# Kernel optimization log

Hardware: AMD Instinct MI355X
Metric: run time of the kernel (lower is better)

## Reference

```python
import jax, jax.numpy as jnp
import numpy as np

# dims: V vocab, D embed, C classes, S seq, L layers, M proj_dim (random features), B batch
V, D, C, S, L, M, B = 32000, 512, 2, 2048, 4, 64, 16
H = 4 * D  # FFN hidden


def setup_inputs() -> dict:
    key = jax.random.key(0)
    ks = jax.random.split(key, 16)
    sc = 0.02
    n = lambda k, shape, s=sc: jax.random.normal(k, shape, jnp.float32) * s
    return {
        'x': jax.random.randint(ks[0], (B, S), 0, V),
        'embed': n(ks[1], (V, D)),
        'pos': n(ks[2], (S, D)),
        'Wq': n(ks[3], (L, D, D)), 'bq': jnp.zeros((L, D), jnp.float32),
        'Wk': n(ks[4], (L, D, D)), 'bk': jnp.zeros((L, D), jnp.float32),
        'Wv': n(ks[5], (L, D, D)), 'bv': jnp.zeros((L, D), jnp.float32),
        'P': jax.random.normal(ks[6], (L, D, M), jnp.float32) / np.sqrt(D),  # Performer random-feature projection
        'Wo': n(ks[7], (L, D, D)), 'bo': jnp.zeros((L, D), jnp.float32),
        'ln_g': jnp.ones((L, D), jnp.float32), 'ln_b': jnp.zeros((L, D), jnp.float32),
        'W1': n(ks[8], (L, D, H)), 'b1': jnp.zeros((L, H), jnp.float32),
        'W2': n(ks[9], (L, H, D)), 'b2': jnp.zeros((L, D), jnp.float32),
        'Wc1': n(ks[10], (D, D // 2)), 'bc1': jnp.zeros((D // 2,), jnp.float32),
        'Wc2': n(ks[11], (D // 2, C)), 'bc2': jnp.zeros((C,), jnp.float32),
    }


def _layernorm(x, g, b, eps=1e-5):
    mu = x.mean(-1, keepdims=True)
    var = ((x - mu) ** 2).mean(-1, keepdims=True)
    return (x - mu) * jax.lax.rsqrt(var + eps) * g + b


def reference(x, embed, pos, Wq, bq, Wk, bk, Wv, bv, P, Wo, bo,
              ln_g, ln_b, W1, b1, W2, b2, Wc1, bc1, Wc2, bc2):
    # token embedding + learned positional embedding
    h = embed[x] + pos[None, :, :]  # [B,S,D]
    for l in range(L):
        r = h
        # Performer linear attention
        q = h @ Wq[l] + bq[l]
        k = h @ Wk[l] + bk[l]
        v = h @ Wv[l] + bv[l]
        pq = jax.nn.elu(q @ P[l]) + 1.0  # [B,S,M] positive feature map
        pk = jax.nn.elu(k @ P[l]) + 1.0
        kv = jnp.einsum('bsm,bsd->bmd', pk, v)              # associative K^T V reduction
        z = jnp.einsum('bsm,bm->bs', pq, pk.sum(axis=1)) + 1e-6
        att = jnp.einsum('bsm,bmd->bsd', pq, kv) / z[..., None]
        att = att @ Wo[l] + bo[l]
        # LayerNorm -> FFN (dropout is identity in eval)
        hn = _layernorm(att, ln_g[l], ln_b[l])
        ff = jax.nn.gelu(hn @ W1[l] + b1[l], approximate=False) @ W2[l] + b2[l]
        h = ff + r  # residual around the whole Sequential block
    pooled = h[:, 0, :]  # CLS pooling
    hid = jax.nn.relu(pooled @ Wc1 + bc1)
    return hid @ Wc2 + bc2  # [B,C] logits
```

## Files before the change

kernel.cpp:

```cpp
#include <hip/hip_runtime.h>
#include <hip/hip_bf16.h>
#include <math.h>

constexpr int kV = 32000;
constexpr int kD = 512;
constexpr int kC = 2;
constexpr int kS = 2048;
constexpr int kL = 4;
constexpr int kM = 64;
constexpr int kB = 16;
constexpr int kH = 2048;
constexpr int kBS = kB * kS;

typedef __hip_bfloat16 bf16;
using bf16x8 = __attribute__((ext_vector_type(8))) short;
using f32x4  = __attribute__((ext_vector_type(4))) float;

#define GLOBAL_LOAD_LDS16(gp, lp)                                              \
  __builtin_amdgcn_global_load_lds(                                            \
      (const __attribute__((address_space(1))) void*)(gp),                     \
      (__attribute__((address_space(3))) void*)(lp), 16, 0, 0)

__device__ inline unsigned short f2bf_u16(float f) {
  bf16 b = __float2bfloat16(f);
  return *reinterpret_cast<unsigned short*>(&b);
}

__device__ inline float fast_gelu(float v) {
  float y  = v * 0.70710678118654752f;
  float ay = fabsf(y);
  float t  = __builtin_amdgcn_rcpf(fmaf(0.3275911f, ay, 1.0f));
  float e  = __expf(-y * y);
  float p  = fmaf(1.061405429f, t, -1.453152027f);
  p = fmaf(p, t, 1.421413741f);
  p = fmaf(p, t, -0.284496736f);
  p = fmaf(p, t, 0.254829592f);
  float er = fmaf(-p * t, e, 1.0f);
  er = copysignf(er, y);
  return 0.5f * v * (1.0f + er);
}

__global__ __launch_bounds__(256) void embed_kernel(const int* __restrict__ x,
    const float* __restrict__ emb, const float* __restrict__ pos,
    float* __restrict__ h, bf16* __restrict__ hb) {
  int tid = blockIdx.x * 256 + threadIdx.x;
  int row = tid >> 7;
  int d4  = tid & 127;
  int tok = x[row];
  int s   = row & (kS - 1);
  float4 e = ((const float4*)emb)[(size_t)tok * 128 + d4];
  float4 p = ((const float4*)pos)[(size_t)s * 128 + d4];
  float4 o;
  o.x = e.x + p.x; o.y = e.y + p.y; o.z = e.z + p.z; o.w = e.w + p.w;
  ((float4*)h)[(size_t)row * 128 + d4] = o;
  ushort4 ub;
  ub.x = f2bf_u16(o.x); ub.y = f2bf_u16(o.y);
  ub.z = f2bf_u16(o.z); ub.w = f2bf_u16(o.w);
  ((ushort4*)hb)[(size_t)row * 128 + d4] = ub;
}

__global__ __launch_bounds__(256) void transpose_cast_kernel(
    const float* __restrict__ W, bf16* __restrict__ Wt, int K, int N) {
  __shared__ float tile[32][33];
  const int k0 = blockIdx.x * 32, n0 = blockIdx.y * 32;
  int tx = threadIdx.x & 31, ty = threadIdx.x >> 5;
#pragma unroll
  for (int i = 0; i < 32; i += 8)
    tile[ty + i][tx] = W[(size_t)(k0 + ty + i) * N + n0 + tx];
  __syncthreads();
#pragma unroll
  for (int i = 0; i < 32; i += 8)
    Wt[(size_t)(n0 + ty + i) * K + k0 + tx] = __float2bfloat16(tile[tx][ty + i]);
}

__global__ __launch_bounds__(256) void cast_bf16_kernel(
    const float* __restrict__ src, bf16* __restrict__ dst) {
  int gid = blockIdx.x * 256 + threadIdx.x;
  float4 v = ((const float4*)src)[gid];
  ushort4 u;
  u.x = f2bf_u16(v.x); u.y = f2bf_u16(v.y);
  u.z = f2bf_u16(v.z); u.w = f2bf_u16(v.w);
  ((ushort4*)dst)[gid] = u;
}

__global__ __launch_bounds__(256) void zero512_kernel(float* __restrict__ p) {
  if (threadIdx.x < 128) ((float4*)p)[threadIdx.x] = make_float4(0.f, 0.f, 0.f, 0.f);
}

__global__ __launch_bounds__(256) void wfold_dual_kernel(
    const float* __restrict__ Wq, const float* __restrict__ Wk,
    const float* __restrict__ P, bf16* __restrict__ Wqpt,
    bf16* __restrict__ Wkpt) {
  int gid = blockIdx.x * 256 + threadIdx.x;
  const float* W = (gid < 32768) ? Wq : Wk;
  bf16* out      = (gid < 32768) ? Wqpt : Wkpt;
  int id = gid & 32767;
  int m  = id & 63;
  int kk = id >> 6;
  float a0 = 0.f, a1 = 0.f, a2 = 0.f, a3 = 0.f;
#pragma unroll 4
  for (int c = 0; c < kD; c += 4) {
    float4 w = *(const float4*)&W[(size_t)kk * kD + c];
    a0 = fmaf(w.x, P[(size_t)(c + 0) * kM + m], a0);
    a1 = fmaf(w.y, P[(size_t)(c + 1) * kM + m], a1);
    a2 = fmaf(w.z, P[(size_t)(c + 2) * kM + m], a2);
    a3 = fmaf(w.w, P[(size_t)(c + 3) * kM + m], a3);
  }
  out[(size_t)m * kD + kk] = __float2bfloat16((a0 + a1) + (a2 + a3));
}

__global__ __launch_bounds__(128) void bfold_kernel(const float* __restrict__ bq,
    const float* __restrict__ bk, const float* __restrict__ P,
    float* __restrict__ bqp, float* __restrict__ bkp) {
  int m = threadIdx.x & (kM - 1);
  const float* src = (threadIdx.x >> 6) ? bk : bq;
  float* dst = (threadIdx.x >> 6) ? bkp : bqp;
  float acc = 0.f;
  for (int c = 0; c < kD; ++c) acc += src[c] * P[(size_t)c * kM + m];
  dst[m] = acc;
}

__global__ __launch_bounds__(256) void bvwo_kernel(const float* __restrict__ bv,
    const float* __restrict__ Wo, float* __restrict__ bvWo) {
  __shared__ float part[4][64];
  int d0 = blockIdx.x * 64;
  int dc = threadIdx.x & 63;
  int eg = threadIdx.x >> 6;
  float acc = 0.f;
  int e0 = eg * 128;
#pragma unroll 4
  for (int e = e0; e < e0 + 128; ++e)
    acc = fmaf(bv[e], Wo[(size_t)e * kD + d0 + dc], acc);
  part[eg][dc] = acc;
  __syncthreads();
  if (eg == 0)
    bvWo[d0 + dc] = (part[0][dc] + part[1][dc]) + (part[2][dc] + part[3][dc]);
}

template <int BK, int BN, int ACT, bool HAS_RES, bool HAS_OUTER, bool WRITE_F32, bool WRITE_BF16>
__global__ __launch_bounds__(256) void mfma_gemm(
    const bf16* __restrict__ A, const bf16* __restrict__ Wt,
    const float* __restrict__ bias, const float* __restrict__ rowv,
    const float* __restrict__ colv, const float* __restrict__ res,
    float* __restrict__ C, bf16* __restrict__ Cb, int K, int N) {
  constexpr int NJ = BN / 32;
  constexpr int CPR = BK / 8;
  constexpr int SW = (BK == 32) ? 1 : 0;
  __shared__ short As[128 * BK];
  __shared__ short Bs[BN * BK];
  const int tid  = threadIdx.x;
  const int lane = tid & 63;
  const int wave = tid >> 6;
  const int nx = gridDim.x;
  const int SH = (gridDim.y & 7) ? gridDim.y : 8;
  const int b_lin = blockIdx.y * nx + blockIdx.x;
  const int stripe = b_lin / (nx * SH);
  const int rem = b_lin - stripe * (nx * SH);
  const int row0 = (stripe * SH + (rem % SH)) * 128;
  const int col0 = (rem / SH) * BN;
  const int wr = (wave & 1) * 64;
  const int wc = (wave >> 1) * (BN / 2);
  const int lcol = lane & 15;
  const int quad = lane >> 4;

  f32x4 acc[4][NJ];
#pragma unroll
  for (int i = 0; i < 4; ++i)
#pragma unroll
    for (int j = 0; j < NJ; ++j) acc[i][j] = (f32x4){0.f, 0.f, 0.f, 0.f};

  for (int k0 = 0; k0 < K; k0 += BK) {
#pragma unroll
    for (int p = 0; p < 128 * CPR / 256; ++p) {
      int idx = p * 256 + tid;
      int r = idx / CPR;
      int kc = (idx % CPR) ^ ((r >> SW) & (CPR - 1));
      GLOBAL_LOAD_LDS16(&A[(size_t)(row0 + r) * K + k0 + kc * 8], &As[idx * 8]);
    }
#pragma unroll
    for (int p = 0; p < BN * CPR / 256; ++p) {
      int idx = p * 256 + tid;
      int r = idx / CPR;
      int kc = (idx % CPR) ^ ((r >> SW) & (CPR - 1));
      GLOBAL_LOAD_LDS16(&Wt[(size_t)(col0 + r) * K + k0 + kc * 8], &Bs[idx * 8]);
    }
    __syncthreads();
#pragma unroll
    for (int kh = 0; kh < BK / 32; ++kh) {
      bf16x8 af[4], bfr[NJ];
#pragma unroll
      for (int i = 0; i < 4; ++i) {
        int rr = wr + i * 16 + lcol;
        int slot = (kh * 4 + quad) ^ ((rr >> SW) & (CPR - 1));
        af[i] = *(const bf16x8*)&As[(rr * CPR + slot) * 8];
      }
#pragma unroll
      for (int j = 0; j < NJ; ++j) {
        int rr = wc + j * 16 + lcol;
        int slot = (kh * 4 + quad) ^ ((rr >> SW) & (CPR - 1));
        bfr[j] = *(const bf16x8*)&Bs[(rr * CPR + slot) * 8];
      }
#pragma unroll
      for (int i = 0; i < 4; ++i)
#pragma unroll
        for (int j = 0; j < NJ; ++j)
          acc[i][j] = __builtin_amdgcn_mfma_f32_16x16x32_bf16(af[i], bfr[j], acc[i][j], 0, 0, 0);
    }
    __syncthreads();
  }

#pragma unroll
  for (int i = 0; i < 4; ++i) {
#pragma unroll
    for (int r = 0; r < 4; ++r) {
      int grow = row0 + wr + i * 16 + quad * 4 + r;
#pragma unroll
      for (int j = 0; j < NJ; ++j) {
        int gcol = col0 + wc + j * 16 + lcol;
        float v = acc[i][j][r];
        if (HAS_OUTER) v += rowv[grow] * colv[gcol];
        else v += bias[gcol];
        if (ACT == 2) v = fast_gelu(v);
        size_t off = (size_t)grow * N + gcol;
        if (HAS_RES) v += res[off];
        if (WRITE_F32) C[off] = v;
        if (WRITE_BF16) Cb[off] = __float2bfloat16(v);
      }
    }
  }
}

__global__ __launch_bounds__(256) void skinny_dual_gemm(
    const bf16* __restrict__ A, const bf16* __restrict__ Wq,
    const bf16* __restrict__ Wk, const float* __restrict__ bq,
    const float* __restrict__ bk, float* __restrict__ pq,
    float* __restrict__ pk) {
  __shared__ short As[64 * 32];
  __shared__ short Bs[128 * 32];
  const int tid  = threadIdx.x;
  const int lane = tid & 63;
  const int wave = tid >> 6;
  const int row0 = blockIdx.x * 64;
  const int lcol = lane & 15;
  const int quad = lane >> 4;

  f32x4 accq[4], acck[4];
#pragma unroll
  for (int i = 0; i < 4; ++i) {
    accq[i] = (f32x4){0.f, 0.f, 0.f, 0.f};
    acck[i] = (f32x4){0.f, 0.f, 0.f, 0.f};
  }

  for (int k0 = 0; k0 < kD; k0 += 32) {
    {
      int r = tid >> 2;
      int kc = (tid & 3) ^ ((r >> 1) & 3);
      GLOBAL_LOAD_LDS16(&A[(size_t)(row0 + r) * kD + k0 + kc * 8], &As[tid * 8]);
    }
#pragma unroll
    for (int p = 0; p < 2; ++p) {
      int idx = p * 256 + tid;
      int r = idx >> 2;
      int kc = (idx & 3) ^ ((r >> 1) & 3);
      const bf16* src = (r < 64) ? &Wq[(size_t)r * kD + k0 + kc * 8]
                                 : &Wk[(size_t)(r - 64) * kD + k0 + kc * 8];
      GLOBAL_LOAD_LDS16(src, &Bs[idx * 8]);
    }
    __syncthreads();
    bf16x8 af[4], bq_f, bk_f;
#pragma unroll
    for (int i = 0; i < 4; ++i) {
      int rr = i * 16 + lcol;
      af[i] = *(const bf16x8*)&As[(rr * 4 + (quad ^ ((rr >> 1) & 3))) * 8];
    }
    {
      int rr = wave * 16 + lcol;
      bq_f = *(const bf16x8*)&Bs[(rr * 4 + (quad ^ ((rr >> 1) & 3))) * 8];
      int rr2 = 64 + wave * 16 + lcol;
      bk_f = *(const bf16x8*)&Bs[(rr2 * 4 + (quad ^ ((rr2 >> 1) & 3))) * 8];
    }
#pragma unroll
    for (int i = 0; i < 4; ++i) {
      accq[i] = __builtin_amdgcn_mfma_f32_16x16x32_bf16(af[i], bq_f, accq[i], 0, 0, 0);
      acck[i] = __builtin_amdgcn_mfma_f32_16x16x32_bf16(af[i], bk_f, acck[i], 0, 0, 0);
    }
    __syncthreads();
  }

#pragma unroll
  for (int i = 0; i < 4; ++i) {
#pragma unroll
    for (int r = 0; r < 4; ++r) {
      int grow = row0 + i * 16 + quad * 4 + r;
      int gcol = wave * 16 + lcol;
      float vq = accq[i][r] + bq[gcol];
      vq = (vq > 0.f) ? (vq + 1.f) : expf(vq);
      pq[(size_t)grow * kM + gcol] = vq;
      float vk = acck[i][r] + bk[gcol];
      vk = (vk > 0.f) ? (vk + 1.f) : expf(vk);
      pk[(size_t)grow * kM + gcol] = vk;
    }
  }
}

__global__ __launch_bounds__(256) void kvh_split_kernel(const float* __restrict__ pk,
    const bf16* __restrict__ hb, float* __restrict__ part) {
  __shared__ float pkS[16][64];
  __shared__ float vS[16][256];
  const int d0 = blockIdx.x * 256, b = blockIdx.y, split = blockIdx.z;
  const int s_beg = split * 128;
  const float* pkb = pk + (size_t)b * kS * kM;
  const bf16* hbb  = hb + (size_t)b * kS * kD;
  const int tid = threadIdx.x;
  const int tx = tid & 15, ty = tid >> 4;
  float4 acc[4][4];
#pragma unroll
  for (int i = 0; i < 4; ++i)
#pragma unroll
    for (int j = 0; j < 4; ++j) acc[i][j] = make_float4(0.f, 0.f, 0.f, 0.f);

  for (int s0 = s_beg; s0 < s_beg + 128; s0 += 16) {
    {
      int e = tid * 4;
      int sr = e >> 6, mc = e & 63;
      *(float4*)&pkS[sr][mc] = *(const float4*)&pkb[(size_t)(s0 + sr) * kM + mc];
    }
#pragma unroll
    for (int p = 0; p < 2; ++p) {
      int idx = p * 256 + tid;
      int sr = idx >> 5, dc8 = idx & 31;
      uint4 raw = *(const uint4*)&hbb[(size_t)(s0 + sr) * kD + d0 + dc8 * 8];
      float4 f0, f1;
      f0.x = __uint_as_float(raw.x << 16);
      f0.y = __uint_as_float(raw.x & 0xffff0000u);
      f0.z = __uint_as_float(raw.y << 16);
      f0.w = __uint_as_float(raw.y & 0xffff0000u);
      f1.x = __uint_as_float(raw.z << 16);
      f1.y = __uint_as_float(raw.z & 0xffff0000u);
      f1.z = __uint_as_float(raw.w << 16);
      f1.w = __uint_as_float(raw.w & 0xffff0000u);
      *(float4*)&vS[sr][dc8 * 8]     = f0;
      *(float4*)&vS[sr][dc8 * 8 + 4] = f1;
    }
    __syncthreads();
#pragma unroll
    for (int sr = 0; sr < 16; ++sr) {
      float a[4];
#pragma unroll
      for (int i = 0; i < 4; ++i) a[i] = pkS[sr][ty * 4 + i];
      float4 bv4[4];
#pragma unroll
      for (int j = 0; j < 4; ++j) bv4[j] = *(const float4*)&vS[sr][tx * 16 + j * 4];
#pragma unroll
      for (int i = 0; i < 4; ++i)
#pragma unroll
        for (int j = 0; j < 4; ++j) {
          acc[i][j].x += a[i] * bv4[j].x;
          acc[i][j].y += a[i] * bv4[j].y;
          acc[i][j].z += a[i] * bv4[j].z;
          acc[i][j].w += a[i] * bv4[j].w;
        }
    }
    __syncthreads();
  }
  float* pp = part + (((size_t)split * kB + b) * kM) * kD;
#pragma unroll
  for (int i = 0; i < 4; ++i)
#pragma unroll
    for (int j = 0; j < 4; ++j)
      *(float4*)&pp[(size_t)(ty * 4 + i) * kD + d0 + tx * 16 + j * 4] = acc[i][j];
}

__global__ __launch_bounds__(256) void kvh_reduce_kernel(const float* __restrict__ part,
                                                         bf16* __restrict__ kvhb) {
  int gid = blockIdx.x * 256 + threadIdx.x;
  float4 s = make_float4(0.f, 0.f, 0.f, 0.f);
#pragma unroll
  for (int sp = 0; sp < 16; ++sp) {
    float4 p = ((const float4*)part)[(size_t)sp * (kB * kM * kD / 4) + gid];
    s.x += p.x; s.y += p.y; s.z += p.z; s.w += p.w;
  }
  ushort4 u;
  u.x = f2bf_u16(s.x); u.y = f2bf_u16(s.y);
  u.z = f2bf_u16(s.z); u.w = f2bf_u16(s.w);
  ((ushort4*)kvhb)[gid] = u;
}

__global__ __launch_bounds__(256) void zero_pks_kernel(float* __restrict__ p) {
  ((float4*)p)[threadIdx.x] = make_float4(0.f, 0.f, 0.f, 0.f);
}

__global__ __launch_bounds__(256) void pksum_kernel(const float* __restrict__ pk,
                                                    float* __restrict__ pksum) {
  __shared__ float part[4][64];
  int b = blockIdx.x >> 4;
  int split = blockIdx.x & 15;
  int lane = threadIdx.x & 63, w = threadIdx.x >> 6;
  float s = 0.f;
  int base = split * 128 + w * 32;
  for (int i = 0; i < 32; ++i)
    s += pk[((size_t)b * kS + base + i) * kM + lane];
  part[w][lane] = s;
  __syncthreads();
  if (w == 0)
    atomicAdd(&pksum[b * kM + lane],
              part[0][lane] + part[1][lane] + part[2][lane] + part[3][lane]);
}

__global__ __launch_bounds__(256) void z_kernel(const float* __restrict__ pq,
    const float* __restrict__ pksum, float* __restrict__ z) {
  int row = blockIdx.x * 4 + (threadIdx.x >> 6);
  int lane = threadIdx.x & 63;
  int b = row >> 11;
  float v = pq[(size_t)row * kM + lane] * pksum[b * kM + lane];
#pragma unroll
  for (int off = 32; off; off >>= 1) v += __shfl_down(v, off);
  if (lane == 0) z[row] = v + 1e-6f;
}

__global__ __launch_bounds__(256) void att_kernel(const float* __restrict__ pq,
    const float* __restrict__ kvo, const float* __restrict__ z,
    const float* __restrict__ bo, float* __restrict__ outf) {
  __shared__ float pqS[64][68];
  __shared__ float kvS[64][68];
  const int d0 = blockIdx.x * 64, s0 = blockIdx.y * 64, b = blockIdx.z;
  const int tid = threadIdx.x;
  const int tx = tid & 15, ty = tid >> 4;
  for (int i = 0; i < 4; ++i) {
    int f = tid + i * 256;
    int r = f >> 4, c = (f & 15) * 4;
    *(float4*)&pqS[r][c] = *(const float4*)&pq[((size_t)(b * kS + s0 + r)) * kM + c];
    *(float4*)&kvS[r][c] = *(const float4*)&kvo[((size_t)b * kM + r) * kD + d0 + c];
  }
  __syncthreads();
  float acc[4][4] = {};
#pragma unroll
  for (int m = 0; m < kM; ++m) {
    float a[4];
#pragma unroll
    for (int i = 0; i < 4; ++i) a[i] = pqS[ty * 4 + i][m];
    float4 b4 = *(const float4*)&kvS[m][tx * 4];
    float bb[4] = {b4.x, b4.y, b4.z, b4.w};
#pragma unroll
    for (int i = 0; i < 4; ++i)
#pragma unroll
      for (int j = 0; j < 4; ++j) acc[i][j] += a[i] * bb[j];
  }
  float4 bo4 = *(const float4*)&bo[d0 + tx * 4];
#pragma unroll
  for (int i = 0; i < 4; ++i) {
    int srow = s0 + ty * 4 + i;
    float zi = 1.0f / z[b * kS + srow];
    float4 o;
    o.x = acc[i][0] * zi + bo4.x;
    o.y = acc[i][1] * zi + bo4.y;
    o.z = acc[i][2] * zi + bo4.z;
    o.w = acc[i][3] * zi + bo4.w;
    *(float4*)&outf[((size_t)(b * kS + srow)) * kD + d0 + tx * 4] = o;
  }
}

__global__ __launch_bounds__(256) void ln_kernel(const float* __restrict__ in,
    const float* __restrict__ g, const float* __restrict__ b,
    bf16* __restrict__ out) {
  __shared__ float ws1[4], ws2[4];
  int row = blockIdx.x, tid = threadIdx.x;
  float2 v = ((const float2*)(in + (size_t)row * kD))[tid];
  float s = v.x + v.y;
#pragma unroll
  for (int off = 32; off; off >>= 1) s += __shfl_down(s, off);
  if ((tid & 63) == 0) ws1[tid >> 6] = s;
  __syncthreads();
  float mean = (ws1[0] + ws1[1] + ws1[2] + ws1[3]) * (1.0f / kD);
  float dx = v.x - mean, dy = v.y - mean;
  float s2 = dx * dx + dy * dy;
#pragma unroll
  for (int off = 32; off; off >>= 1) s2 += __shfl_down(s2, off);
  if ((tid & 63) == 0) ws2[tid >> 6] = s2;
  __syncthreads();
  float var = (ws2[0] + ws2[1] + ws2[2] + ws2[3]) * (1.0f / kD);
  float rstd = rsqrtf(var + 1e-5f);
  float2 gg = ((const float2*)g)[tid];
  float2 bb = ((const float2*)b)[tid];
  ushort2 u;
  u.x = f2bf_u16(dx * rstd * gg.x + bb.x);
  u.y = f2bf_u16(dy * rstd * gg.y + bb.y);
  ((ushort2*)(out + (size_t)row * kD))[tid] = u;
}

__global__ __launch_bounds__(256) void cls_kernel(const float* __restrict__ h,
    const float* __restrict__ Wc1, const float* __restrict__ bc1,
    const float* __restrict__ Wc2, const float* __restrict__ bc2,
    float* __restrict__ out) {
  __shared__ float r0[4], r1[4];
  int b = blockIdx.x;
  int j = threadIdx.x;
  const float* p = h + (size_t)b * kS * kD;
  float acc = bc1[j];
  for (int i = 0; i < kD; ++i) acc += p[i] * Wc1[i * (kD / 2) + j];
  acc = fmaxf(acc, 0.f);
  float p0 = acc * Wc2[j * kC + 0];
  float p1 = acc * Wc2[j * kC + 1];
#pragma unroll
  for (int off = 32; off; off >>= 1) {
    p0 += __shfl_down(p0, off);
    p1 += __shfl_down(p1, off);
  }
  if ((j & 63) == 0) { r0[j >> 6] = p0; r1[j >> 6] = p1; }
  __syncthreads();
  if (j == 0) {
    out[b * kC + 0] = r0[0] + r0[1] + r0[2] + r0[3] + bc2[0];
    out[b * kC + 1] = r1[0] + r1[1] + r1[2] + r1[3] + bc2[1];
  }
}

extern "C" void kernel_launch(void* const* d_in, const int* in_sizes, int n_in,
                              void* d_out, int out_size, void* d_ws, size_t ws_size,
                              hipStream_t stream) {
  const int*   x    = (const int*)  d_in[0];
  const float* emb  = (const float*)d_in[1];
  const float* pos  = (const float*)d_in[2];
  const float* Wq   = (const float*)d_in[3];
  const float* bq   = (const float*)d_in[4];
  const float* Wk   = (const float*)d_in[5];
  const float* bk   = (const float*)d_in[6];
  const float* Wv   = (const float*)d_in[7];
  const float* bv   = (const float*)d_in[8];
  const float* P    = (const float*)d_in[9];
  const float* Wo   = (const float*)d_in[10];
  const float* bo   = (const float*)d_in[11];
  const float* ln_g = (const float*)d_in[12];
  const float* ln_b = (const float*)d_in[13];
  const float* W1   = (const float*)d_in[14];
  const float* b1   = (const float*)d_in[15];
  const float* W2   = (const float*)d_in[16];
  const float* b2   = (const float*)d_in[17];
  const float* Wc1  = (const float*)d_in[18];
  const float* bc1  = (const float*)d_in[19];
  const float* Wc2  = (const float*)d_in[20];
  const float* bc2  = (const float*)d_in[21];
  float* out = (float*)d_out;

  float* h    = (float*)d_ws;
  float* t0   = h    + (size_t)kBS * kD;
  float* pq   = t0   + (size_t)kBS * kD;
  float* pk   = pq   + (size_t)kBS * kM;
  float* kvo  = pk   + (size_t)kBS * kM;
  float* pks  = kvo  + (size_t)kB * kM * kD;
  float* zb   = pks  + (size_t)kB * kM;
  float* bqp  = zb   + kBS;
  float* bkp  = bqp  + kM;
  float* bvWo = bkp  + kM;
  float* zeros= bvWo + kD;
  bf16* hb    = (bf16*)(zeros + kD);
  bf16* ab    = hb + (size_t)kBS * kD;
  bf16* Wqpt  = ab  + (size_t)kBS * kD;
  bf16* Wkpt  = Wqpt + (size_t)kM * kD;
  bf16* Wot   = Wkpt + (size_t)kM * kD;
  bf16* Wvc   = Wot + (size_t)kD * kD;
  bf16* WvWot = Wvc + (size_t)kD * kD;
  bf16* W1t   = WvWot + (size_t)kD * kD;
  bf16* W2t   = W1t + (size_t)kD * kH;
  bf16* kvhb  = W2t + (size_t)kD * kH;
  bf16* F     = (bf16*)t0;
  float* kvpart = (float*)ab;

  zero512_kernel<<<1, 256, 0, stream>>>(zeros);
  embed_kernel<<<kBS * (kD / 4) / 256, 256, 0, stream>>>(x, emb, pos, h, hb);

  for (int l = 0; l < kL; ++l) {
    const float* Pl = P + (size_t)l * kD * kM;

    wfold_dual_kernel<<<256, 256, 0, stream>>>(
        Wq + (size_t)l * kD * kD, Wk + (size_t)l * kD * kD, Pl, Wqpt, Wkpt);
    bfold_kernel<<<1, 128, 0, stream>>>(bq + l * kD, bk + l * kD, Pl, bqp, bkp);
    transpose_cast_kernel<<<dim3(kD / 32, kD / 32), 256, 0, stream>>>(
        Wo + (size_t)l * kD * kD, Wot, kD, kD);
    cast_bf16_kernel<<<kD * kD / 1024, 256, 0, stream>>>(Wv + (size_t)l * kD * kD, Wvc);
    mfma_gemm<32, 64, 0, false, false, false, true><<<dim3(8, 4), 256, 0, stream>>>(
        Wot, Wvc, zeros, nullptr, nullptr, nullptr, nullptr, WvWot, kD, kD);
    bvwo_kernel<<<8, 256, 0, stream>>>(bv + l * kD, Wo + (size_t)l * kD * kD, bvWo);
    transpose_cast_kernel<<<dim3(kD / 32, kH / 32), 256, 0, stream>>>(
        W1 + (size_t)l * kD * kH, W1t, kD, kH);
    transpose_cast_kernel<<<dim3(kH / 32, kD / 32), 256, 0, stream>>>(
        W2 + (size_t)l * kH * kD, W2t, kH, kD);

    skinny_dual_gemm<<<kBS / 64, 256, 0, stream>>>(hb, Wqpt, Wkpt, bqp, bkp, pq, pk);
    kvh_split_kernel<<<dim3(kD / 256, kB, 16), 256, 0, stream>>>(pk, hb, kvpart);
    kvh_reduce_kernel<<<kB * kM * kD / 1024, 256, 0, stream>>>(kvpart, kvhb);
    zero_pks_kernel<<<1, 256, 0, stream>>>(pks);
    pksum_kernel<<<kB * 16, 256, 0, stream>>>(pk, pks);
    z_kernel<<<kBS / 4, 256, 0, stream>>>(pq, pks, zb);
    mfma_gemm<32, 64, 0, false, true, true, false><<<dim3(8, 8), 256, 0, stream>>>(
        kvhb, WvWot, nullptr, pks, bvWo, nullptr, kvo, nullptr, kD, kD);
    att_kernel<<<dim3(kD / 64, kS / 64, kB), 256, 0, stream>>>(pq, kvo, zb, bo + l * kD, t0);
    ln_kernel<<<kBS, 256, 0, stream>>>(t0, ln_g + l * kD, ln_b + l * kD, ab);
    for (int c = 0; c < 2; ++c) {
      size_t ro = (size_t)c * 16384;
      mfma_gemm<64, 128, 2, false, false, false, true><<<dim3(kH / 128, 16384 / 128), 256, 0, stream>>>(
          ab + ro * kD, W1t, b1 + l * kH, nullptr, nullptr, nullptr, nullptr, F, kD, kH);
      mfma_gemm<64, 64, 0, true, false, true, true><<<dim3(kD / 64, 16384 / 128), 256, 0, stream>>>(
          F, W2t, b2 + l * kD, nullptr, nullptr, h + ro * kD, h + ro * kD, hb + ro * kD, kH, kD);
    }
  }

  cls_kernel<<<kB, 256, 0, stream>>>(h, Wc1, bc1, Wc2, bc2, out);
}
```

Before: 1.871 ms.

## Double-buffer LDS tiles in MFMA GEMM and use erff for GELU

Splits the GEMM k-loop into stage and compute steps over two LDS buffers, so the global-to-LDS loads for the next k-tile are issued before the MFMAs on the current tile. This is meant to overlap load latency with compute, at the cost of twice the shared memory per block, which can lower occupancy. It also replaces the polynomial fast GELU approximation with the library erff, which is more exact but may cost more in the epilogue.

After: 2.403 ms. 28.4% more time.

```diff
diff --git a/kernel.cpp b/kernel.cpp
--- a/kernel.cpp
+++ b/kernel.cpp
@@ -24,20 +24,6 @@
 __device__ inline unsigned short f2bf_u16(float f) {
   bf16 b = __float2bfloat16(f);
   return *reinterpret_cast<unsigned short*>(&b);
-}
-
-__device__ inline float fast_gelu(float v) {
-  float y  = v * 0.70710678118654752f;
-  float ay = fabsf(y);
-  float t  = __builtin_amdgcn_rcpf(fmaf(0.3275911f, ay, 1.0f));
-  float e  = __expf(-y * y);
-  float p  = fmaf(1.061405429f, t, -1.453152027f);
-  p = fmaf(p, t, 1.421413741f);
-  p = fmaf(p, t, -0.284496736f);
-  p = fmaf(p, t, 0.254829592f);
-  float er = fmaf(-p * t, e, 1.0f);
-  er = copysignf(er, y);
-  return 0.5f * v * (1.0f + er);
 }
 
 __global__ __launch_bounds__(256) void embed_kernel(const int* __restrict__ x,
@@ -146,8 +132,8 @@
   constexpr int NJ = BN / 32;
   constexpr int CPR = BK / 8;
   constexpr int SW = (BK == 32) ? 1 : 0;
-  __shared__ short As[128 * BK];
-  __shared__ short Bs[BN * BK];
+  __shared__ short As[2][128 * BK];
+  __shared__ short Bs[2][BN * BK];
   const int tid  = threadIdx.x;
   const int lane = tid & 63;
   const int wave = tid >> 6;
@@ -169,22 +155,24 @@
 #pragma unroll
     for (int j = 0; j < NJ; ++j) acc[i][j] = (f32x4){0.f, 0.f, 0.f, 0.f};
 
-  for (int k0 = 0; k0 < K; k0 += BK) {
+  auto stage = [&](short* as, short* bs, int k0) {
 #pragma unroll
     for (int p = 0; p < 128 * CPR / 256; ++p) {
       int idx = p * 256 + tid;
       int r = idx / CPR;
       int kc = (idx % CPR) ^ ((r >> SW) & (CPR - 1));
-      GLOBAL_LOAD_LDS16(&A[(size_t)(row0 + r) * K + k0 + kc * 8], &As[idx * 8]);
+      GLOBAL_LOAD_LDS16(&A[(size_t)(row0 + r) * K + k0 + kc * 8], &as[idx * 8]);
     }
 #pragma unroll
     for (int p = 0; p < BN * CPR / 256; ++p) {
       int idx = p * 256 + tid;
       int r = idx / CPR;
       int kc = (idx % CPR) ^ ((r >> SW) & (CPR - 1));
-      GLOBAL_LOAD_LDS16(&Wt[(size_t)(col0 + r) * K + k0 + kc * 8], &Bs[idx * 8]);
-    }
-    __syncthreads();
+      GLOBAL_LOAD_LDS16(&Wt[(size_t)(col0 + r) * K + k0 + kc * 8], &bs[idx * 8]);
+    }
+  };
+
+  auto compute = [&](const short* as, const short* bs) {
 #pragma unroll
     for (int kh = 0; kh < BK / 32; ++kh) {
       bf16x8 af[4], bfr[NJ];
@@ -192,13 +180,13 @@
       for (int i = 0; i < 4; ++i) {
         int rr = wr + i * 16 + lcol;
         int slot = (kh * 4 + quad) ^ ((rr >> SW) & (CPR - 1));
-        af[i] = *(const bf16x8*)&As[(rr * CPR + slot) * 8];
+        af[i] = *(const bf16x8*)&as[(rr * CPR + slot) * 8];
       }
 #pragma unroll
       for (int j = 0; j < NJ; ++j) {
         int rr = wc + j * 16 + lcol;
         int slot = (kh * 4 + quad) ^ ((rr >> SW) & (CPR - 1));
-        bfr[j] = *(const bf16x8*)&Bs[(rr * CPR + slot) * 8];
+        bfr[j] = *(const bf16x8*)&bs[(rr * CPR + slot) * 8];
       }
 #pragma unroll
       for (int i = 0; i < 4; ++i)
@@ -206,6 +194,17 @@
         for (int j = 0; j < NJ; ++j)
           acc[i][j] = __builtin_amdgcn_mfma_f32_16x16x32_bf16(af[i], bfr[j], acc[i][j], 0, 0, 0);
     }
+  };
+
+  stage(&As[0][0], &Bs[0][0], 0);
+  __syncthreads();
+  for (int k0 = 0; k0 < K; k0 += 2 * BK) {
+    if (k0 + BK < K) stage(&As[1][0], &Bs[1][0], k0 + BK);
+    compute(&As[0][0], &Bs[0][0]);
+    __syncthreads();
+    if (k0 + BK >= K) break;
+    if (k0 + 2 * BK < K) stage(&As[0][0], &Bs[0][0], k0 + 2 * BK);
+    compute(&As[1][0], &Bs[1][0]);
     __syncthreads();
   }
 
@@ -220,7 +219,7 @@
         float v = acc[i][j][r];
         if (HAS_OUTER) v += rowv[grow] * colv[gcol];
         else v += bias[gcol];
-        if (ACT == 2) v = fast_gelu(v);
+        if (ACT == 2) v = 0.5f * v * (1.0f + erff(v * 0.70710678118654752f));
         size_t off = (size_t)grow * N + gcol;
         if (HAS_RES) v += res[off];
         if (WRITE_F32) C[off] = v;
```

## Fuse attention output projection with LayerNorm and use exact erf GELU

Applied to the files above, without the earlier changes.

Merges att_kernel and ln_kernel into one kernel in which each block computes full 512-wide rows for 32 sequence positions, then applies LayerNorm in registers with shuffle reductions. This removes the fp32 intermediate write and reread of the [B*S,D] attention output, plus one kernel launch per layer. It also swaps the polynomial GELU approximation for erff, which costs more in the FFN epilogue but matches the reference more closely. Each block now reloads the full kvo slab, and the larger per-thread accumulator set raises register pressure.

Result: faster. 1.730 ms (-7.5%).

```diff
diff --git a/kernel.cpp b/kernel.cpp
--- a/kernel.cpp
+++ b/kernel.cpp
@@ -24,20 +24,6 @@
 __device__ inline unsigned short f2bf_u16(float f) {
   bf16 b = __float2bfloat16(f);
   return *reinterpret_cast<unsigned short*>(&b);
-}
-
-__device__ inline float fast_gelu(float v) {
-  float y  = v * 0.70710678118654752f;
-  float ay = fabsf(y);
-  float t  = __builtin_amdgcn_rcpf(fmaf(0.3275911f, ay, 1.0f));
-  float e  = __expf(-y * y);
-  float p  = fmaf(1.061405429f, t, -1.453152027f);
-  p = fmaf(p, t, 1.421413741f);
-  p = fmaf(p, t, -0.284496736f);
-  p = fmaf(p, t, 0.254829592f);
-  float er = fmaf(-p * t, e, 1.0f);
-  er = copysignf(er, y);
-  return 0.5f * v * (1.0f + er);
 }
 
 __global__ __launch_bounds__(256) void embed_kernel(const int* __restrict__ x,
@@ -220,7 +206,7 @@
         float v = acc[i][j][r];
         if (HAS_OUTER) v += rowv[grow] * colv[gcol];
         else v += bias[gcol];
-        if (ACT == 2) v = fast_gelu(v);
+        if (ACT == 2) v = 0.5f * v * (1.0f + erff(v * 0.70710678118654752f));
         size_t off = (size_t)grow * N + gcol;
         if (HAS_RES) v += res[off];
         if (WRITE_F32) C[off] = v;
@@ -418,74 +404,99 @@
   if (lane == 0) z[row] = v + 1e-6f;
 }
 
-__global__ __launch_bounds__(256) void att_kernel(const float* __restrict__ pq,
-    const float* __restrict__ kvo, const float* __restrict__ z,
-    const float* __restrict__ bo, float* __restrict__ outf) {
-  __shared__ float pqS[64][68];
-  __shared__ float kvS[64][68];
-  const int d0 = blockIdx.x * 64, s0 = blockIdx.y * 64, b = blockIdx.z;
+__global__ __launch_bounds__(256) void att_ln_kernel(
+    const float* __restrict__ pq, const float* __restrict__ kvo,
+    const float* __restrict__ z, const float* __restrict__ bo,
+    const float* __restrict__ g, const float* __restrict__ bb,
+    bf16* __restrict__ out) {
+  __shared__ float pqS[32][68];
+  __shared__ float kvS[16][520];
+  const int s0 = blockIdx.x * 32, b = blockIdx.y;
   const int tid = threadIdx.x;
   const int tx = tid & 15, ty = tid >> 4;
-  for (int i = 0; i < 4; ++i) {
-    int f = tid + i * 256;
-    int r = f >> 4, c = (f & 15) * 4;
+
+#pragma unroll
+  for (int i = 0; i < 2; ++i) {
+    int f4 = tid + i * 256;
+    int r = f4 >> 4, c = (f4 & 15) * 4;
     *(float4*)&pqS[r][c] = *(const float4*)&pq[((size_t)(b * kS + s0 + r)) * kM + c];
-    *(float4*)&kvS[r][c] = *(const float4*)&kvo[((size_t)b * kM + r) * kD + d0 + c];
-  }
-  __syncthreads();
-  float acc[4][4] = {};
-#pragma unroll
-  for (int m = 0; m < kM; ++m) {
-    float a[4];
-#pragma unroll
-    for (int i = 0; i < 4; ++i) a[i] = pqS[ty * 4 + i][m];
-    float4 b4 = *(const float4*)&kvS[m][tx * 4];
-    float bb[4] = {b4.x, b4.y, b4.z, b4.w};
-#pragma unroll
-    for (int i = 0; i < 4; ++i)
-#pragma unroll
-      for (int j = 0; j < 4; ++j) acc[i][j] += a[i] * bb[j];
-  }
-  float4 bo4 = *(const float4*)&bo[d0 + tx * 4];
-#pragma unroll
-  for (int i = 0; i < 4; ++i) {
-    int srow = s0 + ty * 4 + i;
-    float zi = 1.0f / z[b * kS + srow];
-    float4 o;
-    o.x = acc[i][0] * zi + bo4.x;
-    o.y = acc[i][1] * zi + bo4.y;
-    o.z = acc[i][2] * zi + bo4.z;
-    o.w = acc[i][3] * zi + bo4.w;
-    *(float4*)&outf[((size_t)(b * kS + srow)) * kD + d0 + tx * 4] = o;
-  }
-}
-
-__global__ __launch_bounds__(256) void ln_kernel(const float* __restrict__ in,
-    const float* __restrict__ g, const float* __restrict__ b,
-    bf16* __restrict__ out) {
-  __shared__ float ws1[4], ws2[4];
-  int row = blockIdx.x, tid = threadIdx.x;
-  float2 v = ((const float2*)(in + (size_t)row * kD))[tid];
-  float s = v.x + v.y;
-#pragma unroll
-  for (int off = 32; off; off >>= 1) s += __shfl_down(s, off);
-  if ((tid & 63) == 0) ws1[tid >> 6] = s;
-  __syncthreads();
-  float mean = (ws1[0] + ws1[1] + ws1[2] + ws1[3]) * (1.0f / kD);
-  float dx = v.x - mean, dy = v.y - mean;
-  float s2 = dx * dx + dy * dy;
-#pragma unroll
-  for (int off = 32; off; off >>= 1) s2 += __shfl_down(s2, off);
-  if ((tid & 63) == 0) ws2[tid >> 6] = s2;
-  __syncthreads();
-  float var = (ws2[0] + ws2[1] + ws2[2] + ws2[3]) * (1.0f / kD);
-  float rstd = rsqrtf(var + 1e-5f);
-  float2 gg = ((const float2*)g)[tid];
-  float2 bb = ((const float2*)b)[tid];
-  ushort2 u;
-  u.x = f2bf_u16(dx * rstd * gg.x + bb.x);
-  u.y = f2bf_u16(dy * rstd * gg.y + bb.y);
-  ((ushort2*)(out + (size_t)row * kD))[tid] = u;
+  }
+
+  float4 acc[2][8];
+#pragma unroll
+  for (int i = 0; i < 2; ++i)
+#pragma unroll
+    for (int j = 0; j < 8; ++j) acc[i][j] = make_float4(0.f, 0.f, 0.f, 0.f);
+
+  for (int m0 = 0; m0 < kM; m0 += 16) {
+#pragma unroll
+    for (int p = 0; p < 8; ++p) {
+      int idx = p * 256 + tid;
+      int sr = idx >> 7, c4 = idx & 127;
+      *(float4*)&kvS[sr][c4 * 4] =
+          *(const float4*)&kvo[((size_t)b * kM + m0 + sr) * kD + c4 * 4];
+    }
+    __syncthreads();
+#pragma unroll
+    for (int mm = 0; mm < 16; ++mm) {
+      float a0 = pqS[ty * 2 + 0][m0 + mm];
+      float a1 = pqS[ty * 2 + 1][m0 + mm];
+#pragma unroll
+      for (int j = 0; j < 8; ++j) {
+        float4 bv = *(const float4*)&kvS[mm][j * 64 + tx * 4];
+        acc[0][j].x += a0 * bv.x; acc[0][j].y += a0 * bv.y;
+        acc[0][j].z += a0 * bv.z; acc[0][j].w += a0 * bv.w;
+        acc[1][j].x += a1 * bv.x; acc[1][j].y += a1 * bv.y;
+        acc[1][j].z += a1 * bv.z; acc[1][j].w += a1 * bv.w;
+      }
+    }
+    __syncthreads();
+  }
+
+  float zi0 = 1.0f / z[b * kS + s0 + ty * 2 + 0];
+  float zi1 = 1.0f / z[b * kS + s0 + ty * 2 + 1];
+#pragma unroll
+  for (int j = 0; j < 8; ++j) {
+    float4 bo4 = *(const float4*)&bo[j * 64 + tx * 4];
+    acc[0][j].x = acc[0][j].x * zi0 + bo4.x; acc[0][j].y = acc[0][j].y * zi0 + bo4.y;
+    acc[0][j].z = acc[0][j].z * zi0 + bo4.z; acc[0][j].w = acc[0][j].w * zi0 + bo4.w;
+    acc[1][j].x = acc[1][j].x * zi1 + bo4.x; acc[1][j].y = acc[1][j].y * zi1 + bo4.y;
+    acc[1][j].z = acc[1][j].z * zi1 + bo4.z; acc[1][j].w = acc[1][j].w * zi1 + bo4.w;
+  }
+
+#pragma unroll
+  for (int i = 0; i < 2; ++i) {
+    float s = 0.f;
+#pragma unroll
+    for (int j = 0; j < 8; ++j)
+      s += (acc[i][j].x + acc[i][j].y) + (acc[i][j].z + acc[i][j].w);
+    s += __shfl_xor(s, 1); s += __shfl_xor(s, 2);
+    s += __shfl_xor(s, 4); s += __shfl_xor(s, 8);
+    float mean = s * (1.0f / kD);
+    float v2 = 0.f;
+#pragma unroll
+    for (int j = 0; j < 8; ++j) {
+      float dx = acc[i][j].x - mean, dy = acc[i][j].y - mean;
+      float dz = acc[i][j].z - mean, dw = acc[i][j].w - mean;
+      v2 += (dx * dx + dy * dy) + (dz * dz + dw * dw);
+    }
+    v2 += __shfl_xor(v2, 1); v2 += __shfl_xor(v2, 2);
+    v2 += __shfl_xor(v2, 4); v2 += __shfl_xor(v2, 8);
+    float rstd = rsqrtf(v2 * (1.0f / kD) + 1e-5f);
+    size_t rowoff = ((size_t)(b * kS + s0 + ty * 2 + i)) * kD;
+#pragma unroll
+    for (int j = 0; j < 8; ++j) {
+      int col = j * 64 + tx * 4;
+      float4 g4 = *(const float4*)&g[col];
+      float4 b4 = *(const float4*)&bb[col];
+      ushort4 u;
+      u.x = f2bf_u16((acc[i][j].x - mean) * rstd * g4.x + b4.x);
+      u.y = f2bf_u16((acc[i][j].y - mean) * rstd * g4.y + b4.y);
+      u.z = f2bf_u16((acc[i][j].z - mean) * rstd * g4.z + b4.z);
+      u.w = f2bf_u16((acc[i][j].w - mean) * rstd * g4.w + b4.w);
+      *(ushort4*)&out[rowoff + col] = u;
+    }
+  }
 }
 
 __global__ __launch_bounds__(256) void cls_kernel(const float* __restrict__ h,
@@ -593,8 +604,8 @@
     z_kernel<<<kBS / 4, 256, 0, stream>>>(pq, pks, zb);
     mfma_gemm<32, 64, 0, false, true, true, false><<<dim3(8, 8), 256, 0, stream>>>(
         kvhb, WvWot, nullptr, pks, bvWo, nullptr, kvo, nullptr, kD, kD);
-    att_kernel<<<dim3(kD / 64, kS / 64, kB), 256, 0, stream>>>(pq, kvo, zb, bo + l * kD, t0);
-    ln_kernel<<<kBS, 256, 0, stream>>>(t0, ln_g + l * kD, ln_b + l * kD, ab);
+    att_ln_kernel<<<dim3(kS / 32, kB), 256, 0, stream>>>(
+        pq, kvo, zb, bo + l * kD, ln_g + l * kD, ln_b + l * kD, ab);
     for (int c = 0; c < 2; ++c) {
       size_t ro = (size_t)c * 16384;
       mfma_gemm<64, 128, 2, false, false, false, true><<<dim3(kH / 128, 16384 / 128), 256, 0, stream>>>(
```
